# Kernel optimization log

Hardware: AMD Instinct MI355X
Metric: run time of the kernel (lower is better)

Reference implementation:

```python
import jax, jax.numpy as jnp
import numpy as np

L, B, D, H = 512, 64, 512, 512
HALF = H // 2


def setup_inputs() -> dict:
    key = jax.random.key(0)
    ks = jax.random.split(key, 10)
    s = 0.05
    return {
        "x": jax.random.normal(ks[0], (L, B, D), jnp.float32),
        "mask": jnp.ones((L, B), jnp.float32),
        "W_ih_f": jax.random.normal(ks[1], (4 * HALF, D), jnp.float32) * s,
        "W_hh_f": jax.random.normal(ks[2], (4 * HALF, HALF), jnp.float32) * s,
        "b_ih_f": jax.random.normal(ks[3], (4 * HALF,), jnp.float32) * s,
        "b_hh_f": jax.random.normal(ks[4], (4 * HALF,), jnp.float32) * s,
        "W_ih_b": jax.random.normal(ks[5], (4 * HALF, D), jnp.float32) * s,
        "W_hh_b": jax.random.normal(ks[6], (4 * HALF, HALF), jnp.float32) * s,
        "b_ih_b": jax.random.normal(ks[7], (4 * HALF,), jnp.float32) * s,
        "b_hh_b": jax.random.normal(ks[8], (4 * HALF,), jnp.float32) * s,
    }


def _lstm_dir(x, mask, W_ih, W_hh, b_ih, b_hh, reverse):
    # Precompute input projection as one big GEMM: [L,B,4*HALF]
    xW = jnp.einsum("lbd,gd->lbg", x, W_ih) + b_ih

    def step(carry, inp):
        h, c = carry
        xw_t, m_t = inp  # [B,4*HALF], [B]
        gates = xw_t + h @ W_hh.T + b_hh
        i, f, g, o = jnp.split(gates, 4, axis=-1)
        c = jax.nn.sigmoid(f) * c + jax.nn.sigmoid(i) * jnp.tanh(g)
        h = jax.nn.sigmoid(o) * jnp.tanh(c)
        m = m_t[:, None]
        h = h * m
        c = c * m
        return (h, c), h

    init = (jnp.zeros((x.shape[1], W_hh.shape[1]), x.dtype),
            jnp.zeros((x.shape[1], W_hh.shape[1]), x.dtype))
    _, hs = jax.lax.scan(step, init, (xW, mask), reverse=reverse)
    return hs  # [L,B,HALF], in original time order


def reference(x, mask, W_ih_f, W_hh_f, b_ih_f, b_hh_f, W_ih_b, W_hh_b, b_ih_b, b_hh_b):
    h_fwd = _lstm_dir(x, mask, W_ih_f, W_hh_f, b_ih_f, b_hh_f, reverse=False)
    h_bwd = _lstm_dir(x, mask, W_ih_b, W_hh_b, b_ih_b, b_hh_b, reverse=True)
    return jnp.concatenate([h_fwd, h_bwd], axis=-1)  # [L,B,H]
```

## Files before the change

### kernel.cpp

```cpp
#include <hip/hip_runtime.h>

#define L_SEQ 512
#define NB    64
#define DDIM  512
#define HHALF 256
#define GG    1024

using f32x4  = __attribute__((ext_vector_type(4))) float;
using bf16x8 = __attribute__((ext_vector_type(8))) short;
using f16x8  = __attribute__((ext_vector_type(8))) _Float16;

__device__ __forceinline__ unsigned short f2bf(float f) {
    unsigned u = __float_as_uint(f);
    u += 0x7fffu + ((u >> 16) & 1u);
    return (unsigned short)(u >> 16);
}
__device__ __forceinline__ float fsigmoid(float x) {
    return 1.0f / (1.0f + __expf(-x));
}
__device__ __forceinline__ float ftanh(float x) {
    return 1.0f - 2.0f / (__expf(2.0f * x) + 1.0f);
}

__device__ __forceinline__ void st_short_wt(unsigned short* p, unsigned int v) {
    asm volatile("global_store_short %0, %1, off sc0 sc1" :: "v"(p), "v"(v) : "memory");
}
__device__ __forceinline__ void st_dword_wt(unsigned int* p, unsigned int v) {
    asm volatile("global_store_dword %0, %1, off sc0 sc1" :: "v"(p), "v"(v) : "memory");
}

__global__ __launch_bounds__(256) void gemm_xwb(
    const float* __restrict__ x,
    const float* __restrict__ Wf, const float* __restrict__ Wb,
    const float* __restrict__ bihf, const float* __restrict__ bhhf,
    const float* __restrict__ bihb, const float* __restrict__ bhhb,
    _Float16* __restrict__ xwb,
    unsigned int* __restrict__ zero_base, int zero_words)
{
    const int dir = blockIdx.z;
    const float* __restrict__ W   = dir ? Wb   : Wf;
    const float* __restrict__ bih = dir ? bihb : bihf;
    const float* __restrict__ bhh = dir ? bhhb : bhhf;

    if (blockIdx.x == 0 && blockIdx.y == 0 && blockIdx.z == 0) {
        for (int i = threadIdx.x; i < zero_words; i += 256)
            st_dword_wt(zero_base + i, 0u);
    }

    const int tid = threadIdx.x;
    const int w   = tid >> 6;
    const int l   = tid & 63;
    const int q   = l >> 4;
    const int c   = l & 15;

    const int m0 = blockIdx.y * 64;
    const int n0 = blockIdx.x * 256 + w * 64;

    const float* xa = x + (size_t)(m0 + c) * DDIM + q * 8;
    const float* wa = W + (size_t)(n0 + c) * DDIM + q * 8;

    f32x4 acc[4][4];
#pragma unroll
    for (int rb = 0; rb < 4; ++rb)
#pragma unroll
        for (int nb = 0; nb < 4; ++nb) {
            f32x4 z; z[0] = 0.f; z[1] = 0.f; z[2] = 0.f; z[3] = 0.f;
            acc[rb][nb] = z;
        }

#pragma unroll 2
    for (int k0 = 0; k0 < DDIM; k0 += 32) {
        f16x8 afrag[4], bfrag[4];
#pragma unroll
        for (int rb = 0; rb < 4; ++rb) {
            const float4* p = (const float4*)(xa + (size_t)rb * 16 * DDIM + k0);
            float4 u0 = p[0], u1 = p[1];
            f16x8 v;
            v[0] = (_Float16)u0.x; v[1] = (_Float16)u0.y;
            v[2] = (_Float16)u0.z; v[3] = (_Float16)u0.w;
            v[4] = (_Float16)u1.x; v[5] = (_Float16)u1.y;
            v[6] = (_Float16)u1.z; v[7] = (_Float16)u1.w;
            afrag[rb] = v;
        }
#pragma unroll
        for (int nb = 0; nb < 4; ++nb) {
            const float4* p = (const float4*)(wa + (size_t)nb * 16 * DDIM + k0);
            float4 u0 = p[0], u1 = p[1];
            f16x8 v;
            v[0] = (_Float16)u0.x; v[1] = (_Float16)u0.y;
            v[2] = (_Float16)u0.z; v[3] = (_Float16)u0.w;
            v[4] = (_Float16)u1.x; v[5] = (_Float16)u1.y;
            v[6] = (_Float16)u1.z; v[7] = (_Float16)u1.w;
            bfrag[nb] = v;
        }
#pragma unroll
        for (int rb = 0; rb < 4; ++rb)
#pragma unroll
            for (int nb = 0; nb < 4; ++nb)
                acc[rb][nb] = __builtin_amdgcn_mfma_f32_16x16x32_f16(
                    afrag[rb], bfrag[nb], acc[rb][nb], 0, 0, 0);
    }

#pragma unroll
    for (int nb = 0; nb < 4; ++nb) {
        const int col = n0 + nb * 16 + c;
        const float bias = bih[col] + bhh[col];
#pragma unroll
        for (int rb = 0; rb < 4; ++rb)
#pragma unroll
            for (int r = 0; r < 4; ++r) {
                const int m = m0 + rb * 16 + q * 4 + r;
                xwb[((size_t)dir * (L_SEQ * NB) + m) * GG + col] =
                    (_Float16)(acc[rb][nb][r] + bias);
            }
    }
}

__global__ __launch_bounds__(256, 1) void lstm_recur(
    const _Float16* __restrict__ xwb,
    const float* __restrict__ Whh_f,
    const float* __restrict__ Whh_b,
    const float* __restrict__ mask,
    float* __restrict__ out,
    unsigned short* __restrict__ Hbuf,
    unsigned int* __restrict__ flags)
{
    const int bid = blockIdx.x;
    const int grp = bid & 7;
    const int dir = grp >> 2;
    const int gb  = grp & 3;
    const int g   = bid >> 3;
    unsigned int* cnt = flags + grp * 32;

    const int tid = threadIdx.x;
    const int w   = tid >> 6;
    const int l   = tid & 63;
    const int q   = l >> 4;
    const int c   = l & 15;

    const int b0 = gb * 16;
    const int j  = 64 * g + 16 * w + c;

    const float* __restrict__ Whh = dir ? Whh_b : Whh_f;
    bf16x8 bfrag[4][8];
#pragma unroll
    for (int t = 0; t < 4; ++t) {
        const int gcol = t * HHALF + j;
#pragma unroll
        for (int kt = 0; kt < 8; ++kt) {
            const float4* wp = (const float4*)(Whh + (size_t)gcol * HHALF + kt * 32 + q * 8);
            float4 w0 = wp[0], w1 = wp[1];
            bf16x8 v;
            v[0] = (short)f2bf(w0.x); v[1] = (short)f2bf(w0.y);
            v[2] = (short)f2bf(w0.z); v[3] = (short)f2bf(w0.w);
            v[4] = (short)f2bf(w1.x); v[5] = (short)f2bf(w1.y);
            v[6] = (short)f2bf(w1.z); v[7] = (short)f2bf(w1.w);
            bfrag[t][kt] = v;
        }
    }

    float cstate[4] = {0.f, 0.f, 0.f, 0.f};

    for (int step = 0; step < L_SEQ; ++step) {
        const int tt = dir ? (L_SEQ - 1 - step) : step;

        float xv[4][4];
        const _Float16* xp = xwb + ((size_t)(dir * L_SEQ + tt) * NB + b0 + q * 4) * GG + j;
#pragma unroll
        for (int t = 0; t < 4; ++t)
#pragma unroll
            for (int r = 0; r < 4; ++r)
                xv[t][r] = (float)xp[(size_t)r * GG + t * HHALF];
        float mv[4];
#pragma unroll
        for (int r = 0; r < 4; ++r) mv[r] = mask[tt * NB + b0 + q * 4 + r];

        {
            const unsigned target = 16u * (unsigned)step;
            while (__hip_atomic_load(cnt, __ATOMIC_RELAXED, __HIP_MEMORY_SCOPE_AGENT) < target) {}
        }

        const unsigned short* __restrict__ Hr =
            Hbuf + (size_t)((step & 1) * 2 + dir) * NB * HHALF;
        unsigned short* __restrict__ Hw =
            Hbuf + (size_t)(((step + 1) & 1) * 2 + dir) * NB * HHALF;

        bf16x8 afrag[8];
        const unsigned short* hp = Hr + (size_t)(b0 + c) * HHALF;
#pragma unroll
        for (int kt = 0; kt < 8; ++kt) {
            const unsigned short* p = hp + kt * 32 + q * 8;
            asm volatile("global_load_dwordx4 %0, %1, off sc0 sc1"
                         : "=&v"(afrag[kt]) : "v"(p));
        }
        asm volatile("s_waitcnt vmcnt(0)" ::: "memory");
        __builtin_amdgcn_sched_barrier(0);

        f32x4 acc[4];
#pragma unroll
        for (int t = 0; t < 4; ++t) {
            f32x4 a; a[0] = xv[t][0]; a[1] = xv[t][1]; a[2] = xv[t][2]; a[3] = xv[t][3];
            acc[t] = a;
        }
#pragma unroll
        for (int kt = 0; kt < 8; ++kt)
#pragma unroll
            for (int t = 0; t < 4; ++t)
                acc[t] = __builtin_amdgcn_mfma_f32_16x16x32_bf16(afrag[kt], bfrag[t][kt], acc[t], 0, 0, 0);

        float hval[4];
#pragma unroll
        for (int r = 0; r < 4; ++r) {
            float gi = acc[0][r], gf = acc[1][r], gg = acc[2][r], go = acc[3][r];
            float cn = fsigmoid(gf) * cstate[r] + fsigmoid(gi) * ftanh(gg);
            float h  = fsigmoid(go) * ftanh(cn);
            float m  = mv[r];
            h  *= m;
            cn *= m;
            cstate[r] = cn;
            hval[r]   = h;
            st_short_wt(Hw + (size_t)(b0 + q * 4 + r) * HHALF + j,
                        (unsigned int)f2bf(h));
        }

        asm volatile("s_waitcnt vmcnt(0)" ::: "memory");
        __builtin_amdgcn_sched_barrier(0);
        if (l == 0)
            __hip_atomic_fetch_add(cnt, 1u, __ATOMIC_RELAXED, __HIP_MEMORY_SCOPE_AGENT);
        __builtin_amdgcn_sched_barrier(0);

#pragma unroll
        for (int r = 0; r < 4; ++r) {
            const int b = b0 + q * 4 + r;
            out[((size_t)tt * NB + b) * (2 * HHALF) + dir * HHALF + j] = hval[r];
        }
    }
}

extern "C" void kernel_launch(void* const* d_in, const int* in_sizes, int n_in,
                              void* d_out, int out_size, void* d_ws, size_t ws_size,
                              hipStream_t stream)
{
    (void)in_sizes; (void)n_in; (void)out_size; (void)ws_size;
    const float* x     = (const float*)d_in[0];
    const float* mask  = (const float*)d_in[1];
    const float* Wih_f = (const float*)d_in[2];
    const float* Whh_f = (const float*)d_in[3];
    const float* bih_f = (const float*)d_in[4];
    const float* bhh_f = (const float*)d_in[5];
    const float* Wih_b = (const float*)d_in[6];
    const float* Whh_b = (const float*)d_in[7];
    const float* bih_b = (const float*)d_in[8];
    const float* bhh_b = (const float*)d_in[9];
    float* out = (float*)d_out;

    const size_t xwb_bytes  = (size_t)2 * L_SEQ * NB * GG * sizeof(_Float16);
    const size_t hbuf_bytes = (size_t)2 * 2 * NB * HHALF * sizeof(unsigned short);
    _Float16*       xwb   = (_Float16*)d_ws;
    unsigned short* Hbuf  = (unsigned short*)((char*)d_ws + xwb_bytes);
    unsigned int*   flags = (unsigned int*)((char*)d_ws + xwb_bytes + hbuf_bytes);

    const int zero_words = (int)((hbuf_bytes + 8 * 32 * sizeof(unsigned int)) / 4);
    hipLaunchKernelGGL(gemm_xwb, dim3(4, 512, 2), dim3(256), 0, stream,
                       x, Wih_f, Wih_b, bih_f, bhh_f, bih_b, bhh_b, xwb,
                       (unsigned int*)Hbuf, zero_words);

    hipLaunchKernelGGL(lstm_recur, dim3(32), dim3(256), 0, stream,
                       xwb, Whh_f, Whh_b, mask, out, Hbuf, flags);
}
```

Baseline: 2.284 ms.

## Replace counter-based step barrier with per-value flag bits embedded in output

Removes the atomic counter barrier and separate bf16 H buffer. Each hidden value is written once as fp32 with its low mantissa bit forced to 1, serving as a ready flag. Consumers poll the previous timestep's output slice until every loaded word has the flag bit set, then convert the values to bf16. The GEMM kernel now zeroes the whole output beforehand so the flags start cleared. This aims to cut the atomic and round-trip barrier latency on the serial recurrence, at the cost of a slightly perturbed output LSB, a wider fp32 read per step, and a full-output zeroing pass.

```diff
diff --git a/kernel.cpp b/kernel.cpp
--- a/kernel.cpp
+++ b/kernel.cpp
@@ -7,6 +7,7 @@
 #define GG    1024
 
 using f32x4  = __attribute__((ext_vector_type(4))) float;
+using u32x4  = __attribute__((ext_vector_type(4))) unsigned int;
 using bf16x8 = __attribute__((ext_vector_type(8))) short;
 using f16x8  = __attribute__((ext_vector_type(8))) _Float16;
 
@@ -22,11 +23,13 @@
     return 1.0f - 2.0f / (__expf(2.0f * x) + 1.0f);
 }
 
-__device__ __forceinline__ void st_short_wt(unsigned short* p, unsigned int v) {
-    asm volatile("global_store_short %0, %1, off sc0 sc1" :: "v"(p), "v"(v) : "memory");
-}
 __device__ __forceinline__ void st_dword_wt(unsigned int* p, unsigned int v) {
     asm volatile("global_store_dword %0, %1, off sc0 sc1" :: "v"(p), "v"(v) : "memory");
+}
+__device__ __forceinline__ unsigned cvt_pk_bf16(unsigned a, unsigned b) {
+    unsigned d;
+    asm("v_cvt_pk_bf16_f32 %0, %1, %2" : "=v"(d) : "v"(a), "v"(b));
+    return d;
 }
 
 __global__ __launch_bounds__(256) void gemm_xwb(
@@ -35,16 +38,18 @@
     const float* __restrict__ bihf, const float* __restrict__ bhhf,
     const float* __restrict__ bihb, const float* __restrict__ bhhb,
     _Float16* __restrict__ xwb,
-    unsigned int* __restrict__ zero_base, int zero_words)
+    float* __restrict__ out_zero)
 {
     const int dir = blockIdx.z;
     const float* __restrict__ W   = dir ? Wb   : Wf;
     const float* __restrict__ bih = dir ? bihb : bihf;
     const float* __restrict__ bhh = dir ? bhhb : bhhf;
 
-    if (blockIdx.x == 0 && blockIdx.y == 0 && blockIdx.z == 0) {
-        for (int i = threadIdx.x; i < zero_words; i += 256)
-            st_dword_wt(zero_base + i, 0u);
+    {
+        const int lb = (blockIdx.z * 512 + blockIdx.y) * 4 + blockIdx.x;
+        float4 z4 = make_float4(0.f, 0.f, 0.f, 0.f);
+        float4* zp = (float4*)out_zero + ((size_t)lb * 256 + threadIdx.x) * 4;
+        zp[0] = z4; zp[1] = z4; zp[2] = z4; zp[3] = z4;
     }
 
     const int tid = threadIdx.x;
@@ -121,16 +126,13 @@
     const float* __restrict__ Whh_f,
     const float* __restrict__ Whh_b,
     const float* __restrict__ mask,
-    float* __restrict__ out,
-    unsigned short* __restrict__ Hbuf,
-    unsigned int* __restrict__ flags)
+    float* __restrict__ out)
 {
     const int bid = blockIdx.x;
     const int grp = bid & 7;
     const int dir = grp >> 2;
     const int gb  = grp & 3;
     const int g   = bid >> 3;
-    unsigned int* cnt = flags + grp * 32;
 
     const int tid = threadIdx.x;
     const int w   = tid >> 6;
@@ -175,26 +177,48 @@
 #pragma unroll
         for (int r = 0; r < 4; ++r) mv[r] = mask[tt * NB + b0 + q * 4 + r];
 
-        {
-            const unsigned target = 16u * (unsigned)step;
-            while (__hip_atomic_load(cnt, __ATOMIC_RELAXED, __HIP_MEMORY_SCOPE_AGENT) < target) {}
-        }
-
-        const unsigned short* __restrict__ Hr =
-            Hbuf + (size_t)((step & 1) * 2 + dir) * NB * HHALF;
-        unsigned short* __restrict__ Hw =
-            Hbuf + (size_t)(((step + 1) & 1) * 2 + dir) * NB * HHALF;
-
         bf16x8 afrag[8];
-        const unsigned short* hp = Hr + (size_t)(b0 + c) * HHALF;
-#pragma unroll
-        for (int kt = 0; kt < 8; ++kt) {
-            const unsigned short* p = hp + kt * 32 + q * 8;
-            asm volatile("global_load_dwordx4 %0, %1, off sc0 sc1"
-                         : "=&v"(afrag[kt]) : "v"(p));
-        }
-        asm volatile("s_waitcnt vmcnt(0)" ::: "memory");
-        __builtin_amdgcn_sched_barrier(0);
+        if (step > 0) {
+            const int ttp = dir ? (L_SEQ - step) : (step - 1);
+            const unsigned* pb = (const unsigned*)out
+                + ((size_t)ttp * NB + b0 + c) * (2 * HHALF) + dir * HHALF + q * 8;
+            u32x4 raw[16];
+#define PLOAD(i, off) asm volatile("global_load_dwordx4 %0, %1, off offset:" #off " sc0 sc1" \
+                                   : "=&v"(raw[i]) : "v"(pb))
+            for (;;) {
+                PLOAD(0, 0);    PLOAD(1, 16);
+                PLOAD(2, 128);  PLOAD(3, 144);
+                PLOAD(4, 256);  PLOAD(5, 272);
+                PLOAD(6, 384);  PLOAD(7, 400);
+                PLOAD(8, 512);  PLOAD(9, 528);
+                PLOAD(10, 640); PLOAD(11, 656);
+                PLOAD(12, 768); PLOAD(13, 784);
+                PLOAD(14, 896); PLOAD(15, 912);
+                asm volatile("s_waitcnt vmcnt(0)" ::: "memory");
+                __builtin_amdgcn_sched_barrier(0);
+                unsigned a = 0xFFFFFFFFu;
+#pragma unroll
+                for (int i = 0; i < 16; ++i)
+                    a &= raw[i][0] & raw[i][1] & raw[i][2] & raw[i][3];
+                if (__all((a & 1u) != 0u)) break;
+            }
+#undef PLOAD
+#pragma unroll
+            for (int kt = 0; kt < 8; ++kt) {
+                union { u32x4 u; bf16x8 h; } cv;
+                cv.u[0] = cvt_pk_bf16(raw[2 * kt][0],     raw[2 * kt][1]);
+                cv.u[1] = cvt_pk_bf16(raw[2 * kt][2],     raw[2 * kt][3]);
+                cv.u[2] = cvt_pk_bf16(raw[2 * kt + 1][0], raw[2 * kt + 1][1]);
+                cv.u[3] = cvt_pk_bf16(raw[2 * kt + 1][2], raw[2 * kt + 1][3]);
+                afrag[kt] = cv.h;
+            }
+        } else {
+#pragma unroll
+            for (int kt = 0; kt < 8; ++kt) {
+                bf16x8 z = {0, 0, 0, 0, 0, 0, 0, 0};
+                afrag[kt] = z;
+            }
+        }
 
         f32x4 acc[4];
 #pragma unroll
@@ -208,7 +232,6 @@
             for (int t = 0; t < 4; ++t)
                 acc[t] = __builtin_amdgcn_mfma_f32_16x16x32_bf16(afrag[kt], bfrag[t][kt], acc[t], 0, 0, 0);
 
-        float hval[4];
 #pragma unroll
         for (int r = 0; r < 4; ++r) {
             float gi = acc[0][r], gf = acc[1][r], gg = acc[2][r], go = acc[3][r];
@@ -218,21 +241,11 @@
             h  *= m;
             cn *= m;
             cstate[r] = cn;
-            hval[r]   = h;
-            st_short_wt(Hw + (size_t)(b0 + q * 4 + r) * HHALF + j,
-                        (unsigned int)f2bf(h));
-        }
-
-        asm volatile("s_waitcnt vmcnt(0)" ::: "memory");
-        __builtin_amdgcn_sched_barrier(0);
-        if (l == 0)
-            __hip_atomic_fetch_add(cnt, 1u, __ATOMIC_RELAXED, __HIP_MEMORY_SCOPE_AGENT);
-        __builtin_amdgcn_sched_barrier(0);
-
-#pragma unroll
-        for (int r = 0; r < 4; ++r) {
             const int b = b0 + q * 4 + r;
-            out[((size_t)tt * NB + b) * (2 * HHALF) + dir * HHALF + j] = hval[r];
+            unsigned val = __float_as_uint(h) | 1u;
+            st_dword_wt((unsigned*)out
+                        + ((size_t)tt * NB + b) * (2 * HHALF) + dir * HHALF + j,
+                        val);
         }
     }
 }
@@ -254,17 +267,11 @@
     const float* bhh_b = (const float*)d_in[9];
     float* out = (float*)d_out;
 
-    const size_t xwb_bytes  = (size_t)2 * L_SEQ * NB * GG * sizeof(_Float16);
-    const size_t hbuf_bytes = (size_t)2 * 2 * NB * HHALF * sizeof(unsigned short);
-    _Float16*       xwb   = (_Float16*)d_ws;
-    unsigned short* Hbuf  = (unsigned short*)((char*)d_ws + xwb_bytes);
-    unsigned int*   flags = (unsigned int*)((char*)d_ws + xwb_bytes + hbuf_bytes);
-
-    const int zero_words = (int)((hbuf_bytes + 8 * 32 * sizeof(unsigned int)) / 4);
+    _Float16* xwb = (_Float16*)d_ws;
+
     hipLaunchKernelGGL(gemm_xwb, dim3(4, 512, 2), dim3(256), 0, stream,
-                       x, Wih_f, Wih_b, bih_f, bhh_f, bih_b, bhh_b, xwb,
-                       (unsigned int*)Hbuf, zero_words);
+                       x, Wih_f, Wih_b, bih_f, bhh_f, bih_b, bhh_b, xwb, out);
 
     hipLaunchKernelGGL(lstm_recur, dim3(32), dim3(256), 0, stream,
-                       xwb, Whh_f, Whh_b, mask, out, Hbuf, flags);
-}
+                       xwb, Whh_f, Whh_b, mask, out);
+}
```

After: 3.284 ms. 1.44x slower.

## Replace cross-block flag sync with per-block LSTM recurrence using LDS hidden state

Applied to the files above, without the earlier changes.

The recurrence moves from 32 blocks that trade hidden state through global memory and atomic counters to 8 blocks of 512 threads. Each block owns one direction and 16 batch rows and keeps the full W_hh slice on chip: part in registers, part in LDS, and part read per step from a pre-swizzled bf16 copy that the GEMM kernel writes. The hidden state is double-buffered in LDS and steps are ordered with __syncthreads, which removes the global spin-wait and the write-through stores on the serial critical path. The cost is that each step's MFMA work now falls on far fewer compute units, and part of the weight operand streams from cache every step. The kernel also requests 144KB of dynamic LDS, which may go beyond per-CU limits.

```diff
diff --git a/kernel.cpp b/kernel.cpp
--- a/kernel.cpp
+++ b/kernel.cpp
@@ -22,29 +22,35 @@
     return 1.0f - 2.0f / (__expf(2.0f * x) + 1.0f);
 }
 
-__device__ __forceinline__ void st_short_wt(unsigned short* p, unsigned int v) {
-    asm volatile("global_store_short %0, %1, off sc0 sc1" :: "v"(p), "v"(v) : "memory");
-}
-__device__ __forceinline__ void st_dword_wt(unsigned int* p, unsigned int v) {
-    asm volatile("global_store_dword %0, %1, off sc0 sc1" :: "v"(p), "v"(v) : "memory");
-}
-
 __global__ __launch_bounds__(256) void gemm_xwb(
     const float* __restrict__ x,
     const float* __restrict__ Wf, const float* __restrict__ Wb,
     const float* __restrict__ bihf, const float* __restrict__ bhhf,
     const float* __restrict__ bihb, const float* __restrict__ bhhb,
+    const float* __restrict__ Whhf, const float* __restrict__ Whhb,
     _Float16* __restrict__ xwb,
-    unsigned int* __restrict__ zero_base, int zero_words)
+    unsigned short* __restrict__ wsc)
 {
     const int dir = blockIdx.z;
     const float* __restrict__ W   = dir ? Wb   : Wf;
     const float* __restrict__ bih = dir ? bihb : bihf;
     const float* __restrict__ bhh = dir ? bhhb : bhhf;
 
-    if (blockIdx.x == 0 && blockIdx.y == 0 && blockIdx.z == 0) {
-        for (int i = threadIdx.x; i < zero_words; i += 256)
-            st_dword_wt(zero_base + i, 0u);
+    if (blockIdx.y == 0) {
+        const float* __restrict__ Whh = dir ? Whhb : Whhf;
+#pragma unroll
+        for (int w2 = 0; w2 < 2; ++w2) {
+            const int wv = blockIdx.x * 2 + w2;
+            const int n  = 56 + wv;
+            unsigned short* dst = wsc + ((size_t)dir * 8 + wv) * 4096;
+            for (int idx = threadIdx.x; idx < 4096; idx += 256) {
+                const int j  = idx & 7;
+                const int cc = (idx >> 3) & 15;
+                const int qq = (idx >> 7) & 3;
+                const int kt = idx >> 9;
+                dst[idx] = f2bf(Whh[(size_t)(n * 16 + cc) * HHALF + kt * 32 + qq * 8 + j]);
+            }
+        }
     }
 
     const int tid = threadIdx.x;
@@ -116,21 +122,17 @@
     }
 }
 
-__global__ __launch_bounds__(256, 1) void lstm_recur(
+__global__ __launch_bounds__(512, 2) void lstm_recur(
     const _Float16* __restrict__ xwb,
     const float* __restrict__ Whh_f,
     const float* __restrict__ Whh_b,
     const float* __restrict__ mask,
-    float* __restrict__ out,
-    unsigned short* __restrict__ Hbuf,
-    unsigned int* __restrict__ flags)
+    const unsigned short* __restrict__ wsc,
+    float* __restrict__ out)
 {
     const int bid = blockIdx.x;
-    const int grp = bid & 7;
-    const int dir = grp >> 2;
-    const int gb  = grp & 3;
-    const int g   = bid >> 3;
-    unsigned int* cnt = flags + grp * 32;
+    const int dir = bid >> 2;
+    const int b0  = (bid & 3) * 16;
 
     const int tid = threadIdx.x;
     const int w   = tid >> 6;
@@ -138,102 +140,132 @@
     const int q   = l >> 4;
     const int c   = l & 15;
 
-    const int b0 = gb * 16;
-    const int j  = 64 * g + 16 * w + c;
+    extern __shared__ char lds_raw[];
+    short* s_h = (short*)lds_raw;
+    short* s_w = (short*)(lds_raw + 16384);
 
     const float* __restrict__ Whh = dir ? Whh_b : Whh_f;
-    bf16x8 bfrag[4][8];
-#pragma unroll
-    for (int t = 0; t < 4; ++t) {
-        const int gcol = t * HHALF + j;
+
+    for (int i = tid; i < 4096; i += 512) s_h[i] = 0;
+
+    const int hoff = q * 128 + c * 8;
+
+    bf16x8 bfrag[5][8];
+#pragma unroll
+    for (int i = 0; i < 5; ++i) {
+        const int n = w + 8 * i;
 #pragma unroll
         for (int kt = 0; kt < 8; ++kt) {
-            const float4* wp = (const float4*)(Whh + (size_t)gcol * HHALF + kt * 32 + q * 8);
-            float4 w0 = wp[0], w1 = wp[1];
+            const float* wp = Whh + (size_t)(n * 16 + c) * HHALF + kt * 32 + q * 8;
+            float4 w0 = ((const float4*)wp)[0], w1 = ((const float4*)wp)[1];
             bf16x8 v;
             v[0] = (short)f2bf(w0.x); v[1] = (short)f2bf(w0.y);
             v[2] = (short)f2bf(w0.z); v[3] = (short)f2bf(w0.w);
             v[4] = (short)f2bf(w1.x); v[5] = (short)f2bf(w1.y);
             v[6] = (short)f2bf(w1.z); v[7] = (short)f2bf(w1.w);
-            bfrag[t][kt] = v;
-        }
-    }
-
-    float cstate[4] = {0.f, 0.f, 0.f, 0.f};
+            bfrag[i][kt] = v;
+        }
+    }
+#pragma unroll
+    for (int s2 = 0; s2 < 2; ++s2) {
+        const int n = w + 8 * (5 + s2);
+#pragma unroll
+        for (int kt = 0; kt < 8; ++kt) {
+            const float* wp = Whh + (size_t)(n * 16 + c) * HHALF + kt * 32 + q * 8;
+            float4 w0 = ((const float4*)wp)[0], w1 = ((const float4*)wp)[1];
+            bf16x8 v;
+            v[0] = (short)f2bf(w0.x); v[1] = (short)f2bf(w0.y);
+            v[2] = (short)f2bf(w0.z); v[3] = (short)f2bf(w0.w);
+            v[4] = (short)f2bf(w1.x); v[5] = (short)f2bf(w1.y);
+            v[6] = (short)f2bf(w1.z); v[7] = (short)f2bf(w1.w);
+            *(bf16x8*)&s_w[(w * 2 + s2) * 4096 + kt * 512 + hoff] = v;
+        }
+    }
+    __syncthreads();
+
+    const unsigned short* sbase = wsc + ((size_t)dir * 8 + w) * 4096 + hoff;
+    const short* swp0 = &s_w[(w * 2 + 0) * 4096 + hoff];
+    const short* swp1 = &s_w[(w * 2 + 1) * 4096 + hoff];
+
+    float cstate[2][4] = {{0.f, 0.f, 0.f, 0.f}, {0.f, 0.f, 0.f, 0.f}};
 
     for (int step = 0; step < L_SEQ; ++step) {
         const int tt = dir ? (L_SEQ - 1 - step) : step;
-
-        float xv[4][4];
-        const _Float16* xp = xwb + ((size_t)(dir * L_SEQ + tt) * NB + b0 + q * 4) * GG + j;
+        const int p  = step & 1;
+
+        const _Float16* xp = xwb + ((size_t)(dir * L_SEQ + tt) * NB + b0 + q * 4) * GG + c;
+        f32x4 acc[8];
+#pragma unroll
+        for (int i = 0; i < 8; ++i) {
+            const int goff = (w + 8 * i) * 16;
+            f32x4 a;
+#pragma unroll
+            for (int r = 0; r < 4; ++r)
+                a[r] = (float)xp[(size_t)r * GG + goff];
+            acc[i] = a;
+        }
+
+        bf16x8 sf[4];
 #pragma unroll
         for (int t = 0; t < 4; ++t)
-#pragma unroll
-            for (int r = 0; r < 4; ++r)
-                xv[t][r] = (float)xp[(size_t)r * GG + t * HHALF];
+            sf[t] = *(const bf16x8*)(sbase + t * 512);
+
         float mv[4];
 #pragma unroll
         for (int r = 0; r < 4; ++r) mv[r] = mask[tt * NB + b0 + q * 4 + r];
 
-        {
-            const unsigned target = 16u * (unsigned)step;
-            while (__hip_atomic_load(cnt, __ATOMIC_RELAXED, __HIP_MEMORY_SCOPE_AGENT) < target) {}
-        }
-
-        const unsigned short* __restrict__ Hr =
-            Hbuf + (size_t)((step & 1) * 2 + dir) * NB * HHALF;
-        unsigned short* __restrict__ Hw =
-            Hbuf + (size_t)(((step + 1) & 1) * 2 + dir) * NB * HHALF;
-
-        bf16x8 afrag[8];
-        const unsigned short* hp = Hr + (size_t)(b0 + c) * HHALF;
-#pragma unroll
-        for (int kt = 0; kt < 8; ++kt) {
-            const unsigned short* p = hp + kt * 32 + q * 8;
-            asm volatile("global_load_dwordx4 %0, %1, off sc0 sc1"
-                         : "=&v"(afrag[kt]) : "v"(p));
-        }
-        asm volatile("s_waitcnt vmcnt(0)" ::: "memory");
-        __builtin_amdgcn_sched_barrier(0);
-
-        f32x4 acc[4];
-#pragma unroll
-        for (int t = 0; t < 4; ++t) {
-            f32x4 a; a[0] = xv[t][0]; a[1] = xv[t][1]; a[2] = xv[t][2]; a[3] = xv[t][3];
-            acc[t] = a;
-        }
-#pragma unroll
-        for (int kt = 0; kt < 8; ++kt)
-#pragma unroll
-            for (int t = 0; t < 4; ++t)
-                acc[t] = __builtin_amdgcn_mfma_f32_16x16x32_bf16(afrag[kt], bfrag[t][kt], acc[t], 0, 0, 0);
-
-        float hval[4];
-#pragma unroll
-        for (int r = 0; r < 4; ++r) {
-            float gi = acc[0][r], gf = acc[1][r], gg = acc[2][r], go = acc[3][r];
-            float cn = fsigmoid(gf) * cstate[r] + fsigmoid(gi) * ftanh(gg);
-            float h  = fsigmoid(go) * ftanh(cn);
-            float m  = mv[r];
-            h  *= m;
-            cn *= m;
-            cstate[r] = cn;
-            hval[r]   = h;
-            st_short_wt(Hw + (size_t)(b0 + q * 4 + r) * HHALF + j,
-                        (unsigned int)f2bf(h));
-        }
-
-        asm volatile("s_waitcnt vmcnt(0)" ::: "memory");
-        __builtin_amdgcn_sched_barrier(0);
-        if (l == 0)
-            __hip_atomic_fetch_add(cnt, 1u, __ATOMIC_RELAXED, __HIP_MEMORY_SCOPE_AGENT);
-        __builtin_amdgcn_sched_barrier(0);
-
-#pragma unroll
-        for (int r = 0; r < 4; ++r) {
-            const int b = b0 + q * 4 + r;
-            out[((size_t)tt * NB + b) * (2 * HHALF) + dir * HHALF + j] = hval[r];
-        }
+        const short* hrd = &s_h[p * 4096 + hoff];
+
+#pragma unroll
+        for (int kt = 0; kt < 4; ++kt) {
+            bf16x8 af = *(const bf16x8*)(hrd + kt * 512);
+#pragma unroll
+            for (int i = 0; i < 5; ++i)
+                acc[i] = __builtin_amdgcn_mfma_f32_16x16x32_bf16(af, bfrag[i][kt], acc[i], 0, 0, 0);
+            bf16x8 b5 = *(const bf16x8*)(swp0 + kt * 512);
+            acc[5] = __builtin_amdgcn_mfma_f32_16x16x32_bf16(af, b5, acc[5], 0, 0, 0);
+            bf16x8 b6 = *(const bf16x8*)(swp1 + kt * 512);
+            acc[6] = __builtin_amdgcn_mfma_f32_16x16x32_bf16(af, b6, acc[6], 0, 0, 0);
+            acc[7] = __builtin_amdgcn_mfma_f32_16x16x32_bf16(af, sf[kt], acc[7], 0, 0, 0);
+        }
+#pragma unroll
+        for (int t = 0; t < 4; ++t)
+            sf[t] = *(const bf16x8*)(sbase + (4 + t) * 512);
+#pragma unroll
+        for (int kt = 4; kt < 8; ++kt) {
+            bf16x8 af = *(const bf16x8*)(hrd + kt * 512);
+#pragma unroll
+            for (int i = 0; i < 5; ++i)
+                acc[i] = __builtin_amdgcn_mfma_f32_16x16x32_bf16(af, bfrag[i][kt], acc[i], 0, 0, 0);
+            bf16x8 b5 = *(const bf16x8*)(swp0 + kt * 512);
+            acc[5] = __builtin_amdgcn_mfma_f32_16x16x32_bf16(af, b5, acc[5], 0, 0, 0);
+            bf16x8 b6 = *(const bf16x8*)(swp1 + kt * 512);
+            acc[6] = __builtin_amdgcn_mfma_f32_16x16x32_bf16(af, b6, acc[6], 0, 0, 0);
+            acc[7] = __builtin_amdgcn_mfma_f32_16x16x32_bf16(af, sf[kt - 4], acc[7], 0, 0, 0);
+        }
+
+        short* hwr = &s_h[(p ^ 1) * 4096];
+#pragma unroll
+        for (int ji = 0; ji < 2; ++ji) {
+            const int jt = w + 8 * ji;
+#pragma unroll
+            for (int r = 0; r < 4; ++r) {
+                float gi = acc[0 + ji][r], gf = acc[2 + ji][r];
+                float gg = acc[4 + ji][r], go = acc[6 + ji][r];
+                float cn = fsigmoid(gf) * cstate[ji][r] + fsigmoid(gi) * ftanh(gg);
+                float h  = fsigmoid(go) * ftanh(cn);
+                float m  = mv[r];
+                h  *= m;
+                cn *= m;
+                cstate[ji][r] = cn;
+                const int bl = q * 4 + r;
+                const int j  = jt * 16 + c;
+                hwr[(j >> 5) * 512 + ((j >> 3) & 3) * 128 + bl * 8 + (j & 7)] = (short)f2bf(h);
+                out[((size_t)tt * NB + b0 + bl) * (2 * HHALF) + dir * HHALF + j] = h;
+            }
+        }
+
+        __syncthreads();
     }
 }
 
@@ -254,17 +286,13 @@
     const float* bhh_b = (const float*)d_in[9];
     float* out = (float*)d_out;
 
-    const size_t xwb_bytes  = (size_t)2 * L_SEQ * NB * GG * sizeof(_Float16);
-    const size_t hbuf_bytes = (size_t)2 * 2 * NB * HHALF * sizeof(unsigned short);
-    _Float16*       xwb   = (_Float16*)d_ws;
-    unsigned short* Hbuf  = (unsigned short*)((char*)d_ws + xwb_bytes);
-    unsigned int*   flags = (unsigned int*)((char*)d_ws + xwb_bytes + hbuf_bytes);
-
-    const int zero_words = (int)((hbuf_bytes + 8 * 32 * sizeof(unsigned int)) / 4);
+    _Float16*       xwb = (_Float16*)d_ws;
+    unsigned short* wsc = (unsigned short*)((char*)d_ws + (size_t)2 * L_SEQ * NB * GG * sizeof(_Float16));
+
     hipLaunchKernelGGL(gemm_xwb, dim3(4, 512, 2), dim3(256), 0, stream,
-                       x, Wih_f, Wih_b, bih_f, bhh_f, bih_b, bhh_b, xwb,
-                       (unsigned int*)Hbuf, zero_words);
-
-    hipLaunchKernelGGL(lstm_recur, dim3(32), dim3(256), 0, stream,
-                       xwb, Whh_f, Whh_b, mask, out, Hbuf, flags);
-}
+                       x, Wih_f, Wih_b, bih_f, bhh_f, bih_b, bhh_b,
+                       Whh_f, Whh_b, xwb, wsc);
+
+    hipLaunchKernelGGL(lstm_recur, dim3(8), dim3(512), 147456, stream,
+                       xwb, Whh_f, Whh_b, mask, wsc, out);
+}
```

Measured after the change: 3.670 ms. +60.7%, slower.
